# Kernel optimization log

Hardware: AMD Instinct MI355X
Metric: run time of the kernel (lower is better)

The kernel has to match this reference:

```python
import jax, jax.numpy as jnp
import numpy as np
import math

SEQ_LEN = 2048
D_MODEL = 512
HEADS = 8
HEAD_DIM = D_MODEL // HEADS
BATCH = 4


def setup_inputs() -> dict:
    key = jax.random.key(0)
    ks = jax.random.split(key, 12)
    s = 0.02
    return {
        "query": jax.random.normal(ks[0], (BATCH, SEQ_LEN, D_MODEL), dtype=jnp.float32),
        "Wq": jax.random.normal(ks[1], (D_MODEL, D_MODEL), dtype=jnp.float32) * s,
        "bq": jnp.zeros((D_MODEL,), dtype=jnp.float32),
        "Wk": jax.random.normal(ks[2], (D_MODEL, D_MODEL), dtype=jnp.float32) * s,
        "bk": jnp.zeros((D_MODEL,), dtype=jnp.float32),
        "Wv": jax.random.normal(ks[3], (D_MODEL, D_MODEL), dtype=jnp.float32) * s,
        "bv": jnp.zeros((D_MODEL,), dtype=jnp.float32),
        "Wp": jax.random.normal(ks[4], (D_MODEL, D_MODEL), dtype=jnp.float32) * s,
        "bp": jnp.zeros((D_MODEL,), dtype=jnp.float32),
        "logit_scale": jnp.full((HEADS, 1, 1), math.log(10.0), dtype=jnp.float32),
        "rpe": jax.random.normal(ks[5], (2 * SEQ_LEN - 1, HEADS), dtype=jnp.float32) * s,
    }


def reference(query, Wq, bq, Wk, bk, Wv, bv, Wp, bp, logit_scale, rpe):
    N, S, D = query.shape
    H = HEADS

    def split_heads(x):
        # reshape(N, S, head_dim, H) then permute(0, 3, 1, 2) -> (N, H, S, head_dim)
        return x.reshape(N, S, D // H, H).transpose(0, 3, 1, 2)

    q = split_heads(query @ Wq.T + bq)
    k = split_heads(query @ Wk.T + bk)  # key defaults to query
    v = split_heads(query @ Wv.T + bv)  # value defaults to key

    attn = jnp.einsum("bhqd,bhkd->bhqk", q, k) / math.sqrt(D)
    scale = jnp.exp(jnp.minimum(logit_scale, math.log(1.0 / 0.01)))  # (H,1,1)
    attn = attn * scale[None]

    # relative position bias: idx[i,j] = i - j + S - 1
    idx = jnp.arange(S)[:, None] - jnp.arange(S)[None, :] + (S - 1)  # (S,S)
    bias = jax.nn.sigmoid(rpe[idx].transpose(2, 0, 1))  # (H,S,S)
    attn = attn + bias[None]

    attn = jax.nn.softmax(attn, axis=-1)
    out = jnp.einsum("bhqk,bhkd->bhqd", attn, v)
    out = out.transpose(0, 2, 1, 3).reshape(N, S, D)
    return out @ Wp.T + bp
```

## Files before the change

kernel.cpp:

```cpp
#include <hip/hip_runtime.h>
#include <math.h>

#define N_B 4
#define SEQ 2048
#define DM  512
#define H_N 8
#define DH  64

typedef unsigned short ushort_t;
typedef __attribute__((ext_vector_type(8))) short short8_t;
typedef __attribute__((ext_vector_type(4))) float float4_t;

#define LOG2E 1.4426950408889634074f

__device__ __forceinline__ ushort_t f2bf(float f) {
    unsigned int x = __float_as_uint(f);
    unsigned int lsb = (x >> 16) & 1u;
    x += 0x7fffu + lsb;
    return (ushort_t)(x >> 16);
}
__device__ __forceinline__ unsigned int cvtpk_bf16(float a, float b) {
    unsigned int r;
    asm("v_cvt_pk_bf16_f32 %0, %1, %2" : "=v"(r) : "v"(a), "v"(b));
    return r;
}
__device__ __forceinline__ float fexp2(float x) {
#if __has_builtin(__builtin_amdgcn_exp2f)
    return __builtin_amdgcn_exp2f(x);
#else
    return exp2f(x);
#endif
}
__device__ __forceinline__ void gload_lds16(const ushort_t* g, ushort_t* l) {
    __builtin_amdgcn_global_load_lds((const __attribute__((address_space(1))) void*)g,
                                     (__attribute__((address_space(3))) void*)l,
                                     16, 0, 0);
}

#define Q4 1048576
#define W4 65536
#define RELN 4095
#define GTABN (H_N * RELN)
__global__ __launch_bounds__(256)
void prep(const float* __restrict__ query,
          const float* __restrict__ Wq, const float* __restrict__ Wk,
          const float* __restrict__ Wv, const float* __restrict__ Wp,
          const float* __restrict__ bq, const float* __restrict__ bk,
          const float* __restrict__ bv, const float* __restrict__ bp,
          const float* __restrict__ rpe,
          ushort_t* __restrict__ q16, ushort_t* __restrict__ w16,
          float* __restrict__ bcat, float* __restrict__ gtab)
{
    int i = blockIdx.x * 256 + threadIdx.x;
    if (i < Q4) {
        float4 x = ((const float4*)query)[i];
        uint2 p;
        p.x = cvtpk_bf16(x.x, x.y);
        p.y = cvtpk_bf16(x.z, x.w);
        ((uint2*)q16)[i] = p;
    } else if (i < Q4 + 4 * W4) {
        int wi = i - Q4;
        int w = wi >> 16;
        const float* W = (w == 0) ? Wq : (w == 1) ? Wk : (w == 2) ? Wv : Wp;
        int gwi = wi & (W4 - 1);
        int c = gwi >> 7;
        int g = gwi & 127;
        float4 x = ((const float4*)W)[gwi];
        uint2 p;
        p.x = cvtpk_bf16(x.x, x.y);
        p.y = cvtpk_bf16(x.z, x.w);
        int c2 = (w < 3) ? (((c & 7) << 6) | (c >> 3)) : c;
        ((uint2*)w16)[w * W4 + c2 * 128 + g] = p;
    } else if (i < Q4 + 4 * W4 + 2048) {
        int bi = i - (Q4 + 4 * W4);
        int seg = bi >> 9;
        int c = bi & 511;
        const float* B = (seg == 0) ? bq : (seg == 1) ? bk : (seg == 2) ? bv : bp;
        int c2 = (seg < 3) ? (((c & 7) << 6) | (c >> 3)) : c;
        bcat[seg * 512 + c2] = B[c];
    } else {
        int gi = i - (Q4 + 4 * W4 + 2048);
        if (gi < GTABN) {
            int h = gi / RELN;
            int rel = gi - h * RELN;
            float4 v;
            #pragma unroll
            for (int c = 0; c < 4; c++) {
                int rr = rel - c;
                if (rr < 0) rr = 0;
                float x = rpe[rr * H_N + h];
                ((float*)&v)[c] = LOG2E / (1.0f + __expf(-x));
            }
            ((float4*)gtab)[gi] = v;
        }
    }
}

template<int MODE>
__global__ __launch_bounds__(256)
void mgemm(const ushort_t* __restrict__ A, const ushort_t* __restrict__ B,
           const float* __restrict__ bias,
           ushort_t* __restrict__ q_o, ushort_t* __restrict__ k_o,
           ushort_t* __restrict__ vt_o, float* __restrict__ p_o)
{
    __shared__ __align__(16) union SM {
        struct { ushort_t A[128][64]; ushort_t B[128][64]; } ab;
        ushort_t C[128][128];
    } sm;
    ushort_t (&As)[128][64] = sm.ab.A;
    ushort_t (&Bs)[128][64] = sm.ab.B;

    const int t     = threadIdx.x;
    const int wid   = t >> 6;
    const int lane  = t & 63;
    const int lan16 = lane & 15;
    const int quad  = lane >> 4;
    const int wm    = (wid & 1) * 64;
    const int wn    = (wid >> 1) * 64;

    const int col0 = blockIdx.x * 128;
    const int row0 = blockIdx.y * 128;

    const int srow = lane >> 3;
    const int gchk = (lane & 7) ^ ((lane >> 3) & 7);
    const ushort_t* gA = A + (size_t)(row0 + wid * 8 + srow) * DM + gchk * 8;
    const ushort_t* gB = B + (size_t)(col0 + wid * 8 + srow) * DM + gchk * 8;

    float4_t acc[4][4];
    #pragma unroll
    for (int i = 0; i < 4; i++)
        #pragma unroll
        for (int j = 0; j < 4; j++) acc[i][j] = (float4_t){0.f, 0.f, 0.f, 0.f};

    const int sw = lan16 & 7;

    for (int k0 = 0; k0 < DM; k0 += 64) {
        __syncthreads();
        #pragma unroll
        for (int j = 0; j < 4; j++) {
            gload_lds16(gA + k0 + (size_t)j * 32 * DM, &As[j * 32 + wid * 8][0]);
            gload_lds16(gB + k0 + (size_t)j * 32 * DM, &Bs[j * 32 + wid * 8][0]);
        }
        asm volatile("s_waitcnt vmcnt(0)" ::: "memory");
        __syncthreads();

        #pragma unroll
        for (int kk = 0; kk < 2; kk++) {
            short8_t af[4], bf[4];
            #pragma unroll
            for (int i = 0; i < 4; i++) {
                af[i] = *(const short8_t*)&As[wm + i * 16 + lan16][((kk * 4 + quad) ^ sw) * 8];
                bf[i] = *(const short8_t*)&Bs[wn + i * 16 + lan16][((kk * 4 + quad) ^ sw) * 8];
            }
            #pragma unroll
            for (int i = 0; i < 4; i++)
                #pragma unroll
                for (int j = 0; j < 4; j++)
                    acc[i][j] = __builtin_amdgcn_mfma_f32_16x16x32_bf16(af[i], bf[j], acc[i][j], 0, 0, 0);
        }
    }

    if (MODE == 1) {
        #pragma unroll
        for (int j = 0; j < 4; j++) {
            int col = col0 + wn + j * 16 + lan16;
            float bv = bias[col];
            #pragma unroll
            for (int i = 0; i < 4; i++) {
                #pragma unroll
                for (int reg = 0; reg < 4; reg++) {
                    int row = row0 + wm + i * 16 + quad * 4 + reg;
                    p_o[(size_t)row * DM + col] = acc[i][j][reg] + bv;
                }
            }
        }
        return;
    }

    const int w = col0 >> 9;
    __syncthreads();

    if (w < 2) {
        #pragma unroll
        for (int j = 0; j < 4; j++) {
            float bv = bias[col0 + wn + j * 16 + lan16];
            #pragma unroll
            for (int i = 0; i < 4; i++)
                #pragma unroll
                for (int reg = 0; reg < 4; reg++)
                    sm.C[wm + i * 16 + quad * 4 + reg][wn + j * 16 + lan16] =
                        f2bf(acc[i][j][reg] + bv);
        }
    } else {
        #pragma unroll
        for (int j = 0; j < 4; j++) {
            float bv = bias[col0 + wn + j * 16 + lan16];
            #pragma unroll
            for (int i = 0; i < 4; i++) {
                uint2 pw;
                pw.x = cvtpk_bf16(acc[i][j][0] + bv, acc[i][j][1] + bv);
                pw.y = cvtpk_bf16(acc[i][j][2] + bv, acc[i][j][3] + bv);
                *(uint2*)&sm.C[wn + j * 16 + lan16][wm + i * 16 + quad * 4] = pw;
            }
        }
    }
    __syncthreads();

    const int n   = row0 >> 11;
    const int s0  = row0 & 2047;
    const int hh0 = (col0 & 511) >> 6;

    if (w < 2) {
        ushort_t* dst = (w == 0) ? q_o : k_o;
        #pragma unroll
        for (int it = 0; it < 8; it++) {
            int ch  = it * 256 + t;
            int s   = ch >> 4;
            int c16 = ch & 15;
            int head = hh0 + (c16 >> 3);
            int dq   = (c16 & 7) * 8;
            size_t a = (((size_t)(n * H_N + head)) * SEQ + (s0 + s)) * DH + dq;
            *(uint4*)(dst + a) = *(const uint4*)&sm.C[s][c16 * 8];
        }
    } else {
        #pragma unroll
        for (int it = 0; it < 8; it++) {
            int ch = it * 256 + t;
            int r  = ch >> 4;
            int sg = ch & 15;
            int head = hh0 + (r >> 6);
            int dh   = r & 63;
            size_t a = (((size_t)(n * H_N + head)) * DH + dh) * SEQ + s0 + sg * 8;
            *(uint4*)(vt_o + a) = *(const uint4*)&sm.C[r][sg * 8];
        }
    }
}

__global__ __launch_bounds__(256)
void attn_k(const ushort_t* __restrict__ qw, const ushort_t* __restrict__ kw,
            const ushort_t* __restrict__ vt, const float* __restrict__ lsc,
            const float* __restrict__ gtab, ushort_t* __restrict__ ctx)
{
    __shared__ __align__(16) ushort_t K_s[2][64][72];
    __shared__ __align__(16) ushort_t VT_s[2][64][72];
    __shared__ __align__(16) unsigned int Pp[4][2][16][36];

    const int t     = threadIdx.x;
    const int wid   = t >> 6;
    const int lane  = t & 63;
    const int lan16 = lane & 15;
    const int quad  = lane >> 4;

    const int h  = blockIdx.x;
    const int qt = blockIdx.y;
    const int n  = blockIdx.z;
    const int q0 = qt * 128;

    const size_t headoff = ((size_t)(n * H_N + h)) * SEQ * DH;
    const ushort_t* qh  = qw + headoff;
    const ushort_t* kh  = kw + headoff;
    const ushort_t* vth = vt + headoff;

    float ls = lsc[h];
    const float lm = 4.60517018598809136804f;
    if (ls > lm) ls = lm;
    const float scale2 = __expf(ls) * 0.04419417382415921757f * LOG2E;

    const int qrow0 = q0 + wid * 32 + lan16;
    const float4* gt = (const float4*)gtab + (size_t)h * RELN + (qrow0 + 2047 - quad * 4);

    short8_t qb[2][2];
    #pragma unroll
    for (int qf = 0; qf < 2; qf++) {
        const ushort_t* src = qh + (size_t)(qrow0 + qf * 16) * DH + quad * 8;
        qb[qf][0] = *(const short8_t*)(src);
        qb[qf][1] = *(const short8_t*)(src + 32);
    }

    float l_run[2] = {0.f, 0.f};
    float4_t o[4][2];
    #pragma unroll
    for (int ds = 0; ds < 4; ds++)
        #pragma unroll
        for (int qf = 0; qf < 2; qf++) o[ds][qf] = (float4_t){0.f, 0.f, 0.f, 0.f};

    const int srow = t >> 2;
    const int sc   = (t & 3) * 16;
    const ushort_t* kbase = kh + (size_t)srow * DH + sc;
    const ushort_t* vbase = vth + (size_t)srow * SEQ + sc;

    uint4 kreg0 = *(const uint4*)(kbase);
    uint4 kreg1 = *(const uint4*)(kbase + 8);
    uint4 vreg0 = *(const uint4*)(vbase);
    uint4 vreg1 = *(const uint4*)(vbase + 8);
    float4 b4c[2][4];
    #pragma unroll
    for (int qf = 0; qf < 2; qf++)
        #pragma unroll
        for (int sub = 0; sub < 4; sub++) b4c[qf][sub] = gt[(qf - sub) * 16];
    *(uint4*)&K_s[0][srow][sc]      = kreg0;
    *(uint4*)&K_s[0][srow][sc + 8]  = kreg1;
    *(uint4*)&VT_s[0][srow][sc]     = vreg0;
    *(uint4*)&VT_s[0][srow][sc + 8] = vreg1;
    __syncthreads();
    int cur = 0;

    for (int j0 = 0; j0 < SEQ; j0 += 64) {
        const bool more = (j0 + 64 < SEQ);
        float4 b4n[2][4];
        if (more) {
            kreg0 = *(const uint4*)(kbase + (size_t)(j0 + 64) * DH);
            kreg1 = *(const uint4*)(kbase + (size_t)(j0 + 64) * DH + 8);
            vreg0 = *(const uint4*)(vbase + (j0 + 64));
            vreg1 = *(const uint4*)(vbase + (j0 + 64) + 8);
            const float4* gtp = gt - (j0 + 64);
            #pragma unroll
            for (int qf = 0; qf < 2; qf++)
                #pragma unroll
                for (int sub = 0; sub < 4; sub++) b4n[qf][sub] = gtp[(qf - sub) * 16];
        }

        float4_t st[4][2];
        #pragma unroll
        for (int sub = 0; sub < 4; sub++) {
            const ushort_t* kp = &K_s[cur][sub * 16 + lan16][quad * 8];
            short8_t ka0 = *(const short8_t*)(kp);
            short8_t ka1 = *(const short8_t*)(kp + 32);
            #pragma unroll
            for (int qf = 0; qf < 2; qf++) {
                float4_t a = (float4_t){0.f, 0.f, 0.f, 0.f};
                a = __builtin_amdgcn_mfma_f32_16x16x32_bf16(ka0, qb[qf][0], a, 0, 0, 0);
                a = __builtin_amdgcn_mfma_f32_16x16x32_bf16(ka1, qb[qf][1], a, 0, 0, 0);
                st[sub][qf] = a;
            }
        }

        #pragma unroll
        for (int qf = 0; qf < 2; qf++) {
            float ps = 0.f;
            #pragma unroll
            for (int sub = 0; sub < 4; sub++) {
                float e0 = fexp2(st[sub][qf][0] * scale2 + b4c[qf][sub].x);
                float e1 = fexp2(st[sub][qf][1] * scale2 + b4c[qf][sub].y);
                float e2 = fexp2(st[sub][qf][2] * scale2 + b4c[qf][sub].z);
                float e3 = fexp2(st[sub][qf][3] * scale2 + b4c[qf][sub].w);
                ps += (e0 + e1) + (e2 + e3);
                uint2 pw;
                pw.x = cvtpk_bf16(e0, e1);
                pw.y = cvtpk_bf16(e2, e3);
                *(uint2*)&Pp[wid][qf][lan16][sub * 8 + quad * 2] = pw;
            }
            l_run[qf] += ps;
        }
        asm volatile("s_waitcnt lgkmcnt(0)" ::: "memory");

        #pragma unroll
        for (int ks = 0; ks < 2; ks++) {
            short8_t pb[2];
            #pragma unroll
            for (int qf = 0; qf < 2; qf++)
                pb[qf] = *(const short8_t*)&Pp[wid][qf][lan16][ks * 16 + quad * 4];
            #pragma unroll
            for (int ds = 0; ds < 4; ds++) {
                short8_t va = *(const short8_t*)&VT_s[cur][ds * 16 + lan16][ks * 32 + quad * 8];
                #pragma unroll
                for (int qf = 0; qf < 2; qf++)
                    o[ds][qf] = __builtin_amdgcn_mfma_f32_16x16x32_bf16(va, pb[qf], o[ds][qf], 0, 0, 0);
            }
        }

        if (more) {
            *(uint4*)&K_s[cur ^ 1][srow][sc]      = kreg0;
            *(uint4*)&K_s[cur ^ 1][srow][sc + 8]  = kreg1;
            *(uint4*)&VT_s[cur ^ 1][srow][sc]     = vreg0;
            *(uint4*)&VT_s[cur ^ 1][srow][sc + 8] = vreg1;
            __syncthreads();
            cur ^= 1;
            #pragma unroll
            for (int qf = 0; qf < 2; qf++)
                #pragma unroll
                for (int sub = 0; sub < 4; sub++) b4c[qf][sub] = b4n[qf][sub];
        }
    }

    #pragma unroll
    for (int qf = 0; qf < 2; qf++) {
        float l = l_run[qf];
        l += __shfl_xor(l, 16);
        l += __shfl_xor(l, 32);
        float inv = 1.0f / l;
        int row = qrow0 + qf * 16;
        size_t base = ((size_t)n * SEQ + row) * DM + h * DH;
        #pragma unroll
        for (int ds = 0; ds < 4; ds++) {
            uint2 p;
            p.x = cvtpk_bf16(o[ds][qf][0] * inv, o[ds][qf][1] * inv);
            p.y = cvtpk_bf16(o[ds][qf][2] * inv, o[ds][qf][3] * inv);
            *(uint2*)(ctx + base + ds * 16 + quad * 4) = p;
        }
    }
}

extern "C" void kernel_launch(void* const* d_in, const int* in_sizes, int n_in,
                              void* d_out, int out_size, void* d_ws, size_t ws_size,
                              hipStream_t stream) {
    const float* query = (const float*)d_in[0];
    const float* Wq  = (const float*)d_in[1];
    const float* bq  = (const float*)d_in[2];
    const float* Wk  = (const float*)d_in[3];
    const float* bk  = (const float*)d_in[4];
    const float* Wv  = (const float*)d_in[5];
    const float* bv  = (const float*)d_in[6];
    const float* Wp  = (const float*)d_in[7];
    const float* bp  = (const float*)d_in[8];
    const float* lsc = (const float*)d_in[9];
    const float* rpe = (const float*)d_in[10];

    const size_t QEL = (size_t)N_B * SEQ * DM;
    const size_t WEL = (size_t)DM * DM;
    char* ws = (char*)d_ws;
    ushort_t* q16  = (ushort_t*)(ws);
    ushort_t* w16  = q16 + QEL;
    float*    bcat = (float*)(w16 + 4 * WEL);
    float*    gtab = bcat + 2048;
    ushort_t* qb   = (ushort_t*)(gtab + 4 * GTABN);
    ushort_t* kb   = qb + QEL;
    ushort_t* vtb  = kb + QEL;
    ushort_t* ctx  = vtb + QEL;

    const int PREPN = Q4 + 4 * W4 + 2048 + GTABN;
    prep<<<(PREPN + 255) / 256, 256, 0, stream>>>(
        query, Wq, Wk, Wv, Wp, bq, bk, bv, bp, rpe, q16, w16, bcat, gtab);

    dim3 g1(1536 / 128, (N_B * SEQ) / 128);
    mgemm<0><<<g1, 256, 0, stream>>>(q16, w16, bcat, qb, kb, vtb, nullptr);

    dim3 ga(H_N, SEQ / 128, N_B);
    attn_k<<<ga, 256, 0, stream>>>(qb, kb, vtb, lsc, gtab, ctx);

    dim3 g2(DM / 128, (N_B * SEQ) / 128);
    mgemm<1><<<g2, 256, 0, stream>>>(ctx, w16 + 3 * WEL, bcat + 1536,
                                     nullptr, nullptr, nullptr, (float*)d_out);
}
```

Before: 188.1 us.

## Load K and V fragments directly from global memory, drop LDS staging

The attention kernel no longer stages K and V^T tiles through double-buffered shared memory with block-wide barriers. Each wave now loads its MFMA operand fragments for K and V^T straight from global memory every iteration, and the bias values are loaded per iteration instead of prefetched. This removes the LDS writes, reads and __syncthreads per tile and frees shared memory, which may allow more blocks per CU. In exchange, each of the four waves fetches the same K/V data separately, relying on cache for reuse, and the software prefetch that hid global latency is gone.

```diff
diff --git a/kernel.cpp b/kernel.cpp
--- a/kernel.cpp
+++ b/kernel.cpp
@@ -241,8 +241,6 @@
             const ushort_t* __restrict__ vt, const float* __restrict__ lsc,
             const float* __restrict__ gtab, ushort_t* __restrict__ ctx)
 {
-    __shared__ __align__(16) ushort_t K_s[2][64][72];
-    __shared__ __align__(16) ushort_t VT_s[2][64][72];
     __shared__ __align__(16) unsigned int Pp[4][2][16][36];
 
     const int t     = threadIdx.x;
@@ -284,53 +282,41 @@
         #pragma unroll
         for (int qf = 0; qf < 2; qf++) o[ds][qf] = (float4_t){0.f, 0.f, 0.f, 0.f};
 
-    const int srow = t >> 2;
-    const int sc   = (t & 3) * 16;
-    const ushort_t* kbase = kh + (size_t)srow * DH + sc;
-    const ushort_t* vbase = vth + (size_t)srow * SEQ + sc;
-
-    uint4 kreg0 = *(const uint4*)(kbase);
-    uint4 kreg1 = *(const uint4*)(kbase + 8);
-    uint4 vreg0 = *(const uint4*)(vbase);
-    uint4 vreg1 = *(const uint4*)(vbase + 8);
-    float4 b4c[2][4];
-    #pragma unroll
-    for (int qf = 0; qf < 2; qf++)
-        #pragma unroll
-        for (int sub = 0; sub < 4; sub++) b4c[qf][sub] = gt[(qf - sub) * 16];
-    *(uint4*)&K_s[0][srow][sc]      = kreg0;
-    *(uint4*)&K_s[0][srow][sc + 8]  = kreg1;
-    *(uint4*)&VT_s[0][srow][sc]     = vreg0;
-    *(uint4*)&VT_s[0][srow][sc + 8] = vreg1;
-    __syncthreads();
-    int cur = 0;
-
+    const ushort_t* kfrag = kh + (size_t)(lan16)*DH + quad * 8;
+    const ushort_t* vfrag = vth + (size_t)(lan16)*SEQ + quad * 8;
+
+    #pragma unroll 1
     for (int j0 = 0; j0 < SEQ; j0 += 64) {
-        const bool more = (j0 + 64 < SEQ);
-        float4 b4n[2][4];
-        if (more) {
-            kreg0 = *(const uint4*)(kbase + (size_t)(j0 + 64) * DH);
-            kreg1 = *(const uint4*)(kbase + (size_t)(j0 + 64) * DH + 8);
-            vreg0 = *(const uint4*)(vbase + (j0 + 64));
-            vreg1 = *(const uint4*)(vbase + (j0 + 64) + 8);
-            const float4* gtp = gt - (j0 + 64);
+        short8_t ka[4][2];
+        #pragma unroll
+        for (int sub = 0; sub < 4; sub++) {
+            const ushort_t* kp = kfrag + (size_t)(j0 + sub * 16) * DH;
+            ka[sub][0] = *(const short8_t*)(kp);
+            ka[sub][1] = *(const short8_t*)(kp + 32);
+        }
+        short8_t va[2][4];
+        #pragma unroll
+        for (int ks = 0; ks < 2; ks++)
+            #pragma unroll
+            for (int ds = 0; ds < 4; ds++)
+                va[ks][ds] = *(const short8_t*)(vfrag + (size_t)(ds * 16) * SEQ + j0 + ks * 32);
+        float4 b4[2][4];
+        {
+            const float4* gtp = gt - j0;
             #pragma unroll
             for (int qf = 0; qf < 2; qf++)
                 #pragma unroll
-                for (int sub = 0; sub < 4; sub++) b4n[qf][sub] = gtp[(qf - sub) * 16];
+                for (int sub = 0; sub < 4; sub++) b4[qf][sub] = gtp[(qf - sub) * 16];
         }
 
         float4_t st[4][2];
         #pragma unroll
         for (int sub = 0; sub < 4; sub++) {
-            const ushort_t* kp = &K_s[cur][sub * 16 + lan16][quad * 8];
-            short8_t ka0 = *(const short8_t*)(kp);
-            short8_t ka1 = *(const short8_t*)(kp + 32);
             #pragma unroll
             for (int qf = 0; qf < 2; qf++) {
                 float4_t a = (float4_t){0.f, 0.f, 0.f, 0.f};
-                a = __builtin_amdgcn_mfma_f32_16x16x32_bf16(ka0, qb[qf][0], a, 0, 0, 0);
-                a = __builtin_amdgcn_mfma_f32_16x16x32_bf16(ka1, qb[qf][1], a, 0, 0, 0);
+                a = __builtin_amdgcn_mfma_f32_16x16x32_bf16(ka[sub][0], qb[qf][0], a, 0, 0, 0);
+                a = __builtin_amdgcn_mfma_f32_16x16x32_bf16(ka[sub][1], qb[qf][1], a, 0, 0, 0);
                 st[sub][qf] = a;
             }
         }
@@ -340,10 +326,10 @@
             float ps = 0.f;
             #pragma unroll
             for (int sub = 0; sub < 4; sub++) {
-                float e0 = fexp2(st[sub][qf][0] * scale2 + b4c[qf][sub].x);
-                float e1 = fexp2(st[sub][qf][1] * scale2 + b4c[qf][sub].y);
-                float e2 = fexp2(st[sub][qf][2] * scale2 + b4c[qf][sub].z);
-                float e3 = fexp2(st[sub][qf][3] * scale2 + b4c[qf][sub].w);
+                float e0 = fexp2(st[sub][qf][0] * scale2 + b4[qf][sub].x);
+                float e1 = fexp2(st[sub][qf][1] * scale2 + b4[qf][sub].y);
+                float e2 = fexp2(st[sub][qf][2] * scale2 + b4[qf][sub].z);
+                float e3 = fexp2(st[sub][qf][3] * scale2 + b4[qf][sub].w);
                 ps += (e0 + e1) + (e2 + e3);
                 uint2 pw;
                 pw.x = cvtpk_bf16(e0, e1);
@@ -362,24 +348,10 @@
                 pb[qf] = *(const short8_t*)&Pp[wid][qf][lan16][ks * 16 + quad * 4];
             #pragma unroll
             for (int ds = 0; ds < 4; ds++) {
-                short8_t va = *(const short8_t*)&VT_s[cur][ds * 16 + lan16][ks * 32 + quad * 8];
                 #pragma unroll
                 for (int qf = 0; qf < 2; qf++)
-                    o[ds][qf] = __builtin_amdgcn_mfma_f32_16x16x32_bf16(va, pb[qf], o[ds][qf], 0, 0, 0);
-            }
-        }
-
-        if (more) {
-            *(uint4*)&K_s[cur ^ 1][srow][sc]      = kreg0;
-            *(uint4*)&K_s[cur ^ 1][srow][sc + 8]  = kreg1;
-            *(uint4*)&VT_s[cur ^ 1][srow][sc]     = vreg0;
-            *(uint4*)&VT_s[cur ^ 1][srow][sc + 8] = vreg1;
-            __syncthreads();
-            cur ^= 1;
-            #pragma unroll
-            for (int qf = 0; qf < 2; qf++)
-                #pragma unroll
-                for (int sub = 0; sub < 4; sub++) b4c[qf][sub] = b4n[qf][sub];
+                    o[ds][qf] = __builtin_amdgcn_mfma_f32_16x16x32_bf16(va[ks][ds], pb[qf], o[ds][qf], 0, 0, 0);
+            }
         }
     }
 
```

Result: slower. 255.8 us (+36.0%).
